# Optimization experiments

Hardware: AMD Instinct MI355X
Metric: run time of the kernel (lower is better)

Reference implementation:

```python
import math
import jax, jax.numpy as jnp
import numpy as np

B, S, HID = 2, 2048, 1024
NH, DQ, DV = 16, 64, 64

def _alibi_bias(n_heads, maxlen):
    # standard ALiBi slopes: 2^(-8*(h+1)/n_heads)
    slopes = jnp.asarray([2.0 ** (-8.0 * (h + 1) / n_heads) for h in range(n_heads)], dtype=jnp.float32)
    pos = jnp.arange(maxlen, dtype=jnp.float32)
    rel = pos[None, :] - pos[:, None]              # [i, j] = j - i  (<= 0 on causal part)
    return slopes[:, None, None] * rel[None]       # [n_heads, maxlen, maxlen]

def setup_inputs() -> dict:
    key = jax.random.key(0)
    ks = jax.random.split(key, 6)
    scale = 0.02
    return {
        "hidden_states": jax.random.normal(ks[0], (B, S, HID), dtype=jnp.float32),
        "attention_mask": jnp.ones((B, S), dtype=jnp.int32),
        "Wq": jax.random.normal(ks[1], (HID, NH * DQ), dtype=jnp.float32) * scale,
        "Wk": jax.random.normal(ks[2], (HID, NH * DQ), dtype=jnp.float32) * scale,
        "Wv": jax.random.normal(ks[3], (HID, NH * DV), dtype=jnp.float32) * scale,
        "Wo": jax.random.normal(ks[4], (NH * DV, HID), dtype=jnp.float32) * scale,
        "bo": jnp.zeros((HID,), dtype=jnp.float32),
        "alibi": _alibi_bias(NH, S),
    }

def reference(hidden_states, attention_mask, Wq, Wk, Wv, Wo, bo, alibi):
    N, t, _ = hidden_states.shape
    # QKV projections (no bias), split into heads: [N, H, t, d]
    q = (hidden_states @ Wq).reshape(N, t, NH, DQ).transpose(0, 2, 1, 3)
    k = (hidden_states @ Wk).reshape(N, t, NH, DQ).transpose(0, 2, 1, 3)
    v = (hidden_states @ Wv).reshape(N, t, NH, DV).transpose(0, 2, 1, 3)
    # raw scores, then ALiBi added BEFORE the 1/sqrt(d) scaling (as in source)
    scores = jnp.einsum("bhid,bhjd->bhij", q, k)
    scores = scores + alibi[None, :, :t, :t]
    scores = scores / math.sqrt(DQ)
    # grok tanh softcap at 30
    scores = 30.0 * jnp.tanh(scores / 30.0)
    # causal + padding masks
    causal = jnp.tril(jnp.ones((t, t), dtype=bool))
    scores = jnp.where(causal[None, None], scores, -jnp.inf)
    pad = (attention_mask != 0)[:, None, None, :]  # [N,1,1,T]
    scores = jnp.where(pad, scores, -jnp.inf)
    probs = jax.nn.softmax(scores, axis=-1)        # dropout p=0.0 (eval)
    ctx = jnp.einsum("bhij,bhjd->bhid", probs, v)
    ctx = ctx.transpose(0, 2, 1, 3).reshape(N, t, NH * DV)
    out = ctx @ Wo + bo
    return out
```

## Files before the change

### kernel.cpp

```cpp
#include <hip/hip_runtime.h>
#include <stdint.h>

#define BB 2
#define SS 2048
#define HID 1024
#define NHEAD 16
#define DHEAD 64
#define MTOT (BB*SS)

typedef float  f32x4  __attribute__((ext_vector_type(4)));
typedef short  s16x8  __attribute__((ext_vector_type(8)));
typedef unsigned short u16x4 __attribute__((ext_vector_type(4)));

#define LOG2E 1.4426950408889634f

__device__ __forceinline__ unsigned short f2bf(float x){
  union { float f; unsigned u; } v; v.f = x;
  unsigned r = v.u + 0x7fffu + ((v.u >> 16) & 1u);
  return (unsigned short)(r >> 16);
}

__device__ __forceinline__ void gl2lds16(const unsigned short* g, unsigned short* l){
  __builtin_amdgcn_global_load_lds((const __attribute__((address_space(1))) void*)g,
                                   (__attribute__((address_space(3))) void*)l, 16, 0, 0);
}

__global__ __launch_bounds__(256) void k_convert_x(const float* __restrict__ x,
                                                   unsigned short* __restrict__ xb){
  int i = blockIdx.x * 256 + threadIdx.x;
  const float4* xp = (const float4*)x;
  float4 v = xp[i];
  u16x4 o; o.x = f2bf(v.x); o.y = f2bf(v.y); o.z = f2bf(v.z); o.w = f2bf(v.w);
  ((u16x4*)xb)[i] = o;
}

__global__ __launch_bounds__(256) void k_convert_w(const float* __restrict__ Wq,
                                                   const float* __restrict__ Wk,
                                                   const float* __restrict__ Wv,
                                                   const float* __restrict__ Wo,
                                                   unsigned short* __restrict__ Wt,
                                                   unsigned short* __restrict__ Wot){
  __shared__ float tile[64][65];
  int z = blockIdx.z;
  const float* src = (z==0) ? Wq : (z==1) ? Wk : (z==2) ? Wv : Wo;
  unsigned short* dst = (z < 3) ? (Wt + z * HID * HID) : Wot;
  int n0 = blockIdx.x * 64, k0 = blockIdx.y * 64;
  int t = threadIdx.x, tx = t & 63, ty = t >> 6;
  #pragma unroll
  for (int i = 0; i < 16; i++){
    int kl = ty + i*4;
    tile[kl][tx] = src[(k0 + kl) * HID + n0 + tx];
  }
  __syncthreads();
  #pragma unroll
  for (int i = 0; i < 16; i++){
    int nl = ty + i*4;
    dst[(n0 + nl) * HID + k0 + tx] = f2bf(tile[tx][nl]);
  }
}

__global__ __launch_bounds__(256) void k_gemm_qkv(const unsigned short* __restrict__ A,
                                                  const unsigned short* __restrict__ Bt,
                                                  unsigned short* __restrict__ Qb,
                                                  unsigned short* __restrict__ Kb,
                                                  unsigned short* __restrict__ Vt){
  __shared__ __align__(16) unsigned short As[128*32];
  __shared__ __align__(16) unsigned short Bs[128*32];
  int t = threadIdx.x;
  int L = t & 63, w = t >> 6;
  int q = L >> 4, c = L & 15;
  int m0 = blockIdx.x * 128, n0 = blockIdx.y * 128;
  int wr = w >> 1, wc = w & 1;
  f32x4 acc[4][4];
  #pragma unroll
  for (int i = 0; i < 4; i++)
    #pragma unroll
    for (int j = 0; j < 4; j++) acc[i][j] = (f32x4){0.f,0.f,0.f,0.f};

  for (int kb = 0; kb < 32; kb++){
    __syncthreads();
    #pragma unroll
    for (int i = 0; i < 2; i++){
      int p = t + i*256;
      int row = p >> 2, cp = p & 3;
      gl2lds16(A  + (m0 + row) * HID + kb*32 + cp*8, As + p*8);
      gl2lds16(Bt + (n0 + row) * HID + kb*32 + cp*8, Bs + p*8);
    }
    __syncthreads();
    s16x8 af[4], bf[4];
    #pragma unroll
    for (int i = 0; i < 4; i++){
      int m = wr*64 + i*16 + c;
      af[i] = *(const s16x8*)(As + m*32 + q*8);
      int n = wc*64 + i*16 + c;
      bf[i] = *(const s16x8*)(Bs + n*32 + q*8);
    }
    #pragma unroll
    for (int i = 0; i < 4; i++)
      #pragma unroll
      for (int j = 0; j < 4; j++)
        acc[i][j] = __builtin_amdgcn_mfma_f32_16x16x32_bf16(af[i], bf[j], acc[i][j], 0, 0, 0);
  }

  int wsel = n0 >> 10;
  #pragma unroll
  for (int i = 0; i < 4; i++){
    #pragma unroll
    for (int j = 0; j < 4; j++){
      int m_l = wr*64 + i*16 + q*4;
      int n_g = n0 + wc*64 + j*16 + c;
      int nw  = n_g & 1023;
      if (wsel == 0){
        #pragma unroll
        for (int r = 0; r < 4; r++)
          Qb[(m0 + m_l + r) * HID + nw] = f2bf(acc[i][j][r] * 0.125f);
      } else if (wsel == 1){
        #pragma unroll
        for (int r = 0; r < 4; r++)
          Kb[(m0 + m_l + r) * HID + nw] = f2bf(acc[i][j][r]);
      } else {
        int tok = m0 + m_l;
        int b = tok >> 11, s = tok & 2047;
        int h = nw >> 6, d = nw & 63;
        u16x4 pk;
        pk.x = f2bf(acc[i][j][0]); pk.y = f2bf(acc[i][j][1]);
        pk.z = f2bf(acc[i][j][2]); pk.w = f2bf(acc[i][j][3]);
        *(u16x4*)(Vt + (((b*NHEAD + h)*DHEAD + d) * (size_t)SS + s)) = pk;
      }
    }
  }
}

__global__ __launch_bounds__(256) void k_attn(const unsigned short* __restrict__ Qb,
                                              const unsigned short* __restrict__ Kb,
                                              const unsigned short* __restrict__ Vt,
                                              const int* __restrict__ amask,
                                              unsigned short* __restrict__ ctx){
  __shared__ __align__(16) unsigned short UQ[4*16*72];
  __shared__ __align__(16) unsigned short Ks[64*64];
  __shared__ __align__(16) unsigned short Vs[64*64];

  int t = threadIdx.x;
  int L = t & 63, w = t >> 6;
  int q = L >> 4, c = L & 15;
  int qt = 31 - (int)blockIdx.x;
  int bh = blockIdx.y;
  int b = bh >> 4, h = bh & 15;
  int i0 = qt * 64;

  int hp = h + 1;
  float slope = (hp & 1) ? 0.70710678118654752f : 1.0f;
  slope = ldexpf(slope, -((hp >> 1) + 3));

  #pragma unroll
  for (int i = 0; i < 2; i++){
    int p = t + i*256; int row = p >> 3, cp = p & 7; int gc = cp ^ (row & 7);
    gl2lds16(Qb + (size_t)(b*SS + i0 + row) * HID + h*DHEAD + gc*8, UQ + p*8);
  }
  __syncthreads();
  s16x8 qf0, qf1;
  {
    int m = w*16 + c;
    qf0 = *(const s16x8*)(UQ + m*64 + ((0 + q) ^ (m & 7)) * 8);
    qf1 = *(const s16x8*)(UQ + m*64 + ((4 + q) ^ (m & 7)) * 8);
  }

  f32x4 cacc[4];
  #pragma unroll
  for (int i = 0; i < 4; i++) cacc[i] = (f32x4){0.f,0.f,0.f,0.f};
  float lrow[4] = {0.f,0.f,0.f,0.f};

  const float C1 = 86.5617024533378f;
  const float C2 = 0.0961796693925976f;

  for (int jt = 0; jt <= qt; jt++){
    int j0 = jt * 64;
    __syncthreads();
    #pragma unroll
    for (int i = 0; i < 2; i++){
      int p = t + i*256; int row = p >> 3, cp = p & 7; int gc = cp ^ (row & 7);
      gl2lds16(Kb + (size_t)(b*SS + j0 + row) * HID + h*DHEAD + gc*8, Ks + p*8);
      gl2lds16(Vt + (size_t)(bh*DHEAD + row) * SS + j0 + gc*8, Vs + p*8);
    }
    __syncthreads();

    f32x4 sacc[4];
    #pragma unroll
    for (int ct = 0; ct < 4; ct++){
      int n = ct*16 + c;
      s16x8 kf0 = *(const s16x8*)(Ks + n*64 + ((0 + q) ^ (n & 7)) * 8);
      s16x8 kf1 = *(const s16x8*)(Ks + n*64 + ((4 + q) ^ (n & 7)) * 8);
      f32x4 z = (f32x4){0.f,0.f,0.f,0.f};
      z = __builtin_amdgcn_mfma_f32_16x16x32_bf16(qf0, kf0, z, 0, 0, 0);
      z = __builtin_amdgcn_mfma_f32_16x16x32_bf16(qf1, kf1, z, 0, 0, 0);
      sacc[ct] = z;
    }

    float p_[4][4];
    #pragma unroll
    for (int ct = 0; ct < 4; ct++){
      int jg = j0 + ct*16 + c;
      int pad = amask[b*SS + jg];
      #pragma unroll
      for (int r = 0; r < 4; r++){
        int ig = i0 + w*16 + q*4 + r;
        float s = sacc[ct][r] + slope * (float)(jg - ig);
        float e2 = exp2f(s * C2);
        float pv = exp2f(-C1 / (e2 + 1.0f));
        bool ok = (jg <= ig) && (pad != 0);
        pv = ok ? pv : 0.0f;
        p_[ct][r] = pv;
        lrow[r] += pv;
      }
    }

    unsigned short* pw = UQ + w * (16*72);
    #pragma unroll
    for (int ct = 0; ct < 4; ct++)
      #pragma unroll
      for (int r = 0; r < 4; r++)
        pw[(q*4 + r)*72 + ct*16 + c] = f2bf(p_[ct][r]);

    s16x8 pf0 = *(const s16x8*)(pw + c*72 + q*8);
    s16x8 pf1 = *(const s16x8*)(pw + c*72 + 32 + q*8);
    #pragma unroll
    for (int nt = 0; nt < 4; nt++){
      int d = nt*16 + c;
      s16x8 vf0 = *(const s16x8*)(Vs + d*64 + ((0 + q) ^ (d & 7)) * 8);
      s16x8 vf1 = *(const s16x8*)(Vs + d*64 + ((4 + q) ^ (d & 7)) * 8);
      cacc[nt] = __builtin_amdgcn_mfma_f32_16x16x32_bf16(pf0, vf0, cacc[nt], 0, 0, 0);
      cacc[nt] = __builtin_amdgcn_mfma_f32_16x16x32_bf16(pf1, vf1, cacc[nt], 0, 0, 0);
    }
  }

  float inv[4];
  #pragma unroll
  for (int r = 0; r < 4; r++){
    float l = lrow[r];
    l += __shfl_xor(l, 1, 64);
    l += __shfl_xor(l, 2, 64);
    l += __shfl_xor(l, 4, 64);
    l += __shfl_xor(l, 8, 64);
    inv[r] = 1.0f / l;
  }
  #pragma unroll
  for (int nt = 0; nt < 4; nt++){
    int d = nt*16 + c;
    #pragma unroll
    for (int r = 0; r < 4; r++){
      int ig = i0 + w*16 + q*4 + r;
      ctx[(size_t)(b*SS + ig) * HID + h*DHEAD + d] = f2bf(cacc[nt][r] * inv[r]);
    }
  }
}

__global__ __launch_bounds__(256) void k_gemm_out(const unsigned short* __restrict__ A,
                                                  const unsigned short* __restrict__ Bt,
                                                  float* __restrict__ out,
                                                  const float* __restrict__ bo){
  __shared__ __align__(16) unsigned short As[128*32];
  __shared__ __align__(16) unsigned short Bs[128*32];
  int t = threadIdx.x;
  int L = t & 63, w = t >> 6;
  int q = L >> 4, c = L & 15;
  int m0 = blockIdx.x * 128, n0 = blockIdx.y * 128;
  int wr = w >> 1, wc = w & 1;
  f32x4 acc[4][4];
  #pragma unroll
  for (int i = 0; i < 4; i++)
    #pragma unroll
    for (int j = 0; j < 4; j++) acc[i][j] = (f32x4){0.f,0.f,0.f,0.f};

  for (int kb = 0; kb < 32; kb++){
    __syncthreads();
    #pragma unroll
    for (int i = 0; i < 2; i++){
      int p = t + i*256;
      int row = p >> 2, cp = p & 3;
      gl2lds16(A  + (m0 + row) * HID + kb*32 + cp*8, As + p*8);
      gl2lds16(Bt + (n0 + row) * HID + kb*32 + cp*8, Bs + p*8);
    }
    __syncthreads();
    s16x8 af[4], bf[4];
    #pragma unroll
    for (int i = 0; i < 4; i++){
      int m = wr*64 + i*16 + c;
      af[i] = *(const s16x8*)(As + m*32 + q*8);
      int n = wc*64 + i*16 + c;
      bf[i] = *(const s16x8*)(Bs + n*32 + q*8);
    }
    #pragma unroll
    for (int i = 0; i < 4; i++)
      #pragma unroll
      for (int j = 0; j < 4; j++)
        acc[i][j] = __builtin_amdgcn_mfma_f32_16x16x32_bf16(af[i], bf[j], acc[i][j], 0, 0, 0);
  }

  #pragma unroll
  for (int j = 0; j < 4; j++){
    int n = n0 + wc*64 + j*16 + c;
    float bv = bo[n];
    #pragma unroll
    for (int i = 0; i < 4; i++){
      int m = m0 + wr*64 + i*16 + q*4;
      #pragma unroll
      for (int r = 0; r < 4; r++)
        out[(size_t)(m + r) * HID + n] = acc[i][j][r] + bv;
    }
  }
}

extern "C" void kernel_launch(void* const* d_in, const int* in_sizes, int n_in,
                              void* d_out, int out_size, void* d_ws, size_t ws_size,
                              hipStream_t stream){
  const float* hs    = (const float*)d_in[0];
  const int*   amask = (const int*)  d_in[1];
  const float* Wq    = (const float*)d_in[2];
  const float* Wk    = (const float*)d_in[3];
  const float* Wv    = (const float*)d_in[4];
  const float* Wo    = (const float*)d_in[5];
  const float* bo    = (const float*)d_in[6];
  float* out = (float*)d_out;

  char* ws = (char*)d_ws;
  unsigned short* Xb  = (unsigned short*)(ws);
  unsigned short* Wt  = (unsigned short*)(ws + (8u  << 20));
  unsigned short* Wot = (unsigned short*)(ws + (14u << 20));
  unsigned short* Qb  = (unsigned short*)(ws + (16u << 20));
  unsigned short* Kb  = (unsigned short*)(ws + (24u << 20));
  unsigned short* Vt  = (unsigned short*)(ws + (32u << 20));
  unsigned short* Ctx = (unsigned short*)(ws + (40u << 20));

  hipLaunchKernelGGL(k_convert_x, dim3(MTOT*HID/4/256), dim3(256), 0, stream, hs, Xb);
  hipLaunchKernelGGL(k_convert_w, dim3(16,16,4), dim3(256), 0, stream, Wq, Wk, Wv, Wo, Wt, Wot);
  hipLaunchKernelGGL(k_gemm_qkv,  dim3(32,24),   dim3(256), 0, stream, Xb, Wt, Qb, Kb, Vt);
  hipLaunchKernelGGL(k_attn,      dim3(32,32),   dim3(256), 0, stream, Qb, Kb, Vt, amask, Ctx);
  hipLaunchKernelGGL(k_gemm_out,  dim3(32,8),    dim3(256), 0, stream, Ctx, Wot, out, bo);
}
```

Before: 555.5 us.

## Split long causal attention rows across two blocks and combine partial sums

The attention grid grows from 32 to 48 query-tile slots per head. The upper 16 query tiles, which have the longest causal key ranges, are each split into two key chunks handled by separate blocks. This balances the work across blocks. Partial numerators and row sums are written to workspace and merged in a new combine kernel that also normalises. The change also moves the V transpose out of the QKV GEMM epilogue into its own kernel, applies the causal mask only on the diagonal tile, and uses a hardware reciprocal. The cost is extra launches, fp32 partial traffic, and bf16 rounding of the unnormalised numerator.

```diff
diff --git a/kernel.cpp b/kernel.cpp
--- a/kernel.cpp
+++ b/kernel.cpp
@@ -18,6 +18,9 @@
   union { float f; unsigned u; } v; v.f = x;
   unsigned r = v.u + 0x7fffu + ((v.u >> 16) & 1u);
   return (unsigned short)(r >> 16);
+}
+__device__ __forceinline__ float bf2f(unsigned short h){
+  union { unsigned u; float f; } v; v.u = ((unsigned)h) << 16; return v.f;
 }
 
 __device__ __forceinline__ void gl2lds16(const unsigned short* g, unsigned short* l){
@@ -63,7 +66,7 @@
                                                   const unsigned short* __restrict__ Bt,
                                                   unsigned short* __restrict__ Qb,
                                                   unsigned short* __restrict__ Kb,
-                                                  unsigned short* __restrict__ Vt){
+                                                  unsigned short* __restrict__ Vb){
   __shared__ __align__(16) unsigned short As[128*32];
   __shared__ __align__(16) unsigned short Bs[128*32];
   int t = threadIdx.x;
@@ -103,31 +106,46 @@
   }
 
   int wsel = n0 >> 10;
+  unsigned short* dst = (wsel==0) ? Qb : (wsel==1) ? Kb : Vb;
+  float scale = (wsel==0) ? 0.125f : 1.0f;
   #pragma unroll
   for (int i = 0; i < 4; i++){
     #pragma unroll
     for (int j = 0; j < 4; j++){
       int m_l = wr*64 + i*16 + q*4;
-      int n_g = n0 + wc*64 + j*16 + c;
-      int nw  = n_g & 1023;
-      if (wsel == 0){
-        #pragma unroll
-        for (int r = 0; r < 4; r++)
-          Qb[(m0 + m_l + r) * HID + nw] = f2bf(acc[i][j][r] * 0.125f);
-      } else if (wsel == 1){
-        #pragma unroll
-        for (int r = 0; r < 4; r++)
-          Kb[(m0 + m_l + r) * HID + nw] = f2bf(acc[i][j][r]);
-      } else {
-        int tok = m0 + m_l;
-        int b = tok >> 11, s = tok & 2047;
-        int h = nw >> 6, d = nw & 63;
-        u16x4 pk;
-        pk.x = f2bf(acc[i][j][0]); pk.y = f2bf(acc[i][j][1]);
-        pk.z = f2bf(acc[i][j][2]); pk.w = f2bf(acc[i][j][3]);
-        *(u16x4*)(Vt + (((b*NHEAD + h)*DHEAD + d) * (size_t)SS + s)) = pk;
-      }
-    }
+      int nw  = (n0 + wc*64 + j*16 + c) & 1023;
+      #pragma unroll
+      for (int r = 0; r < 4; r++)
+        dst[(m0 + m_l + r) * HID + nw] = f2bf(acc[i][j][r] * scale);
+    }
+  }
+}
+
+__global__ __launch_bounds__(256) void k_transpose_v(const unsigned short* __restrict__ Vb,
+                                                     unsigned short* __restrict__ Vt){
+  __shared__ unsigned tile[64][33];
+  int st = blockIdx.x, bh = blockIdx.y;
+  int b = bh >> 4, h = bh & 15;
+  int t = threadIdx.x;
+  int lr = t >> 4, lc = t & 15;
+  #pragma unroll
+  for (int i = 0; i < 4; i++){
+    int sl = lr + i*16;
+    u16x4 v = *(const u16x4*)(Vb + (size_t)(b*SS + st*64 + sl) * HID + h*DHEAD + lc*4);
+    tile[sl][lc*2]     = (unsigned)v.x | ((unsigned)v.y << 16);
+    tile[sl][lc*2 + 1] = (unsigned)v.z | ((unsigned)v.w << 16);
+  }
+  __syncthreads();
+  #pragma unroll
+  for (int i = 0; i < 4; i++){
+    int dl = lr + i*16;
+    int sh = (dl & 1) * 16, dw = dl >> 1;
+    u16x4 o;
+    o.x = (unsigned short)(tile[lc*4 + 0][dw] >> sh);
+    o.y = (unsigned short)(tile[lc*4 + 1][dw] >> sh);
+    o.z = (unsigned short)(tile[lc*4 + 2][dw] >> sh);
+    o.w = (unsigned short)(tile[lc*4 + 3][dw] >> sh);
+    *(u16x4*)(Vt + (size_t)(bh*DHEAD + dl) * SS + st*64 + lc*4) = o;
   }
 }
 
@@ -135,7 +153,10 @@
                                               const unsigned short* __restrict__ Kb,
                                               const unsigned short* __restrict__ Vt,
                                               const int* __restrict__ amask,
-                                              unsigned short* __restrict__ ctx){
+                                              unsigned short* __restrict__ NumBf,
+                                              float* __restrict__ Lsum,
+                                              float* __restrict__ Part2,
+                                              float* __restrict__ L2){
   __shared__ __align__(16) unsigned short UQ[4*16*72];
   __shared__ __align__(16) unsigned short Ks[64*64];
   __shared__ __align__(16) unsigned short Vs[64*64];
@@ -143,9 +164,21 @@
   int t = threadIdx.x;
   int L = t & 63, w = t >> 6;
   int q = L >> 4, c = L & 15;
-  int qt = 31 - (int)blockIdx.x;
+  int x = blockIdx.x;
   int bh = blockIdx.y;
   int b = bh >> 4, h = bh & 15;
+
+  int qt, jt0, jt1, chunk1;
+  if (x < 32){
+    qt = 31 - (x >> 1);
+    int h0 = (qt + 1) >> 1;
+    chunk1 = x & 1;
+    jt0 = chunk1 ? h0 : 0;
+    jt1 = chunk1 ? (qt + 1) : h0;
+  } else {
+    qt = 47 - x;
+    jt0 = 0; jt1 = qt + 1; chunk1 = 0;
+  }
   int i0 = qt * 64;
 
   int hp = h + 1;
@@ -165,6 +198,10 @@
     qf1 = *(const s16x8*)(UQ + m*64 + ((4 + q) ^ (m & 7)) * 8);
   }
 
+  float si[4];
+  #pragma unroll
+  for (int r = 0; r < 4; r++) si[r] = slope * (float)(i0 + w*16 + q*4 + r);
+
   f32x4 cacc[4];
   #pragma unroll
   for (int i = 0; i < 4; i++) cacc[i] = (f32x4){0.f,0.f,0.f,0.f};
@@ -173,7 +210,7 @@
   const float C1 = 86.5617024533378f;
   const float C2 = 0.0961796693925976f;
 
-  for (int jt = 0; jt <= qt; jt++){
+  for (int jt = jt0; jt < jt1; jt++){
     int j0 = jt * 64;
     __syncthreads();
     #pragma unroll
@@ -200,19 +237,31 @@
     #pragma unroll
     for (int ct = 0; ct < 4; ct++){
       int jg = j0 + ct*16 + c;
-      int pad = amask[b*SS + jg];
+      float padf = (amask[b*SS + jg] != 0) ? 1.0f : 0.0f;
+      float sjg = slope * (float)jg;
       #pragma unroll
       for (int r = 0; r < 4; r++){
-        int ig = i0 + w*16 + q*4 + r;
-        float s = sacc[ct][r] + slope * (float)(jg - ig);
+        float s = sacc[ct][r] + (sjg - si[r]);
         float e2 = exp2f(s * C2);
-        float pv = exp2f(-C1 / (e2 + 1.0f));
-        bool ok = (jg <= ig) && (pad != 0);
-        pv = ok ? pv : 0.0f;
-        p_[ct][r] = pv;
-        lrow[r] += pv;
+        float pv = exp2f(-C1 * __builtin_amdgcn_rcpf(e2 + 1.0f));
+        p_[ct][r] = pv * padf;
       }
     }
+    if (jt == qt){
+      #pragma unroll
+      for (int ct = 0; ct < 4; ct++){
+        int jg = j0 + ct*16 + c;
+        #pragma unroll
+        for (int r = 0; r < 4; r++){
+          int ig = i0 + w*16 + q*4 + r;
+          if (jg > ig) p_[ct][r] = 0.0f;
+        }
+      }
+    }
+    #pragma unroll
+    for (int ct = 0; ct < 4; ct++)
+      #pragma unroll
+      for (int r = 0; r < 4; r++) lrow[r] += p_[ct][r];
 
     unsigned short* pw = UQ + w * (16*72);
     #pragma unroll
@@ -233,7 +282,7 @@
     }
   }
 
-  float inv[4];
+  float lred[4];
   #pragma unroll
   for (int r = 0; r < 4; r++){
     float l = lrow[r];
@@ -241,17 +290,67 @@
     l += __shfl_xor(l, 2, 64);
     l += __shfl_xor(l, 4, 64);
     l += __shfl_xor(l, 8, 64);
-    inv[r] = 1.0f / l;
-  }
-  #pragma unroll
-  for (int nt = 0; nt < 4; nt++){
-    int d = nt*16 + c;
-    #pragma unroll
-    for (int r = 0; r < 4; r++){
-      int ig = i0 + w*16 + q*4 + r;
-      ctx[(size_t)(b*SS + ig) * HID + h*DHEAD + d] = f2bf(cacc[nt][r] * inv[r]);
-    }
-  }
+    lred[r] = l;
+  }
+
+  if (!chunk1){
+    #pragma unroll
+    for (int nt = 0; nt < 4; nt++){
+      int d = nt*16 + c;
+      #pragma unroll
+      for (int r = 0; r < 4; r++){
+        int ig = i0 + w*16 + q*4 + r;
+        NumBf[(size_t)(b*SS + ig) * HID + h*DHEAD + d] = f2bf(cacc[nt][r]);
+      }
+    }
+    if (c == 0){
+      #pragma unroll
+      for (int r = 0; r < 4; r++)
+        Lsum[bh*SS + i0 + w*16 + q*4 + r] = lred[r];
+    }
+  } else {
+    int slot = bh*16 + (qt - 16);
+    float* pn = Part2 + (size_t)slot * 64 * 64;
+    #pragma unroll
+    for (int nt = 0; nt < 4; nt++){
+      int d = nt*16 + c;
+      #pragma unroll
+      for (int r = 0; r < 4; r++){
+        int row = w*16 + q*4 + r;
+        pn[row*64 + d] = cacc[nt][r];
+      }
+    }
+    if (c == 0){
+      #pragma unroll
+      for (int r = 0; r < 4; r++)
+        L2[slot*64 + w*16 + q*4 + r] = lred[r];
+    }
+  }
+}
+
+__global__ __launch_bounds__(256) void k_combine(unsigned short* __restrict__ NumBf,
+                                                 const float* __restrict__ Lsum,
+                                                 const float* __restrict__ Part2,
+                                                 const float* __restrict__ L2){
+  int idx = blockIdx.x * 256 + threadIdx.x;
+  int tok = idx >> 8;
+  int hd4 = (idx & 255) * 4;
+  int h = hd4 >> 6, d0 = hd4 & 63;
+  int b = tok >> 11, i = tok & 2047;
+  int bh = b*16 + h, qt = i >> 6;
+  u16x4 nv = *(u16x4*)(NumBf + (size_t)tok * HID + hd4);
+  float n0 = bf2f(nv.x), n1 = bf2f(nv.y), n2 = bf2f(nv.z), n3 = bf2f(nv.w);
+  float l = Lsum[bh*SS + i];
+  if (qt >= 16){
+    int slot = bh*16 + (qt - 16);
+    const float* pn = Part2 + ((size_t)slot * 64 + (i & 63)) * 64 + d0;
+    n0 += pn[0]; n1 += pn[1]; n2 += pn[2]; n3 += pn[3];
+    l += L2[slot*64 + (i & 63)];
+  }
+  float rl = __builtin_amdgcn_rcpf(l);
+  u16x4 o;
+  o.x = f2bf(n0*rl); o.y = f2bf(n1*rl); o.z = f2bf(n2*rl); o.w = f2bf(n3*rl);
+  *(u16x4*)(NumBf + (size_t)tok * HID + hd4) = o;
 }
 
 __global__ __launch_bounds__(256) void k_gemm_out(const unsigned short* __restrict__ A,
@@ -330,10 +429,17 @@
   unsigned short* Kb  = (unsigned short*)(ws + (24u << 20));
   unsigned short* Vt  = (unsigned short*)(ws + (32u << 20));
   unsigned short* Ctx = (unsigned short*)(ws + (40u << 20));
-
-  hipLaunchKernelGGL(k_convert_x, dim3(MTOT*HID/4/256), dim3(256), 0, stream, hs, Xb);
-  hipLaunchKernelGGL(k_convert_w, dim3(16,16,4), dim3(256), 0, stream, Wq, Wk, Wv, Wo, Wt, Wot);
-  hipLaunchKernelGGL(k_gemm_qkv,  dim3(32,24),   dim3(256), 0, stream, Xb, Wt, Qb, Kb, Vt);
-  hipLaunchKernelGGL(k_attn,      dim3(32,32),   dim3(256), 0, stream, Qb, Kb, Vt, amask, Ctx);
-  hipLaunchKernelGGL(k_gemm_out,  dim3(32,8),    dim3(256), 0, stream, Ctx, Wot, out, bo);
-}
+  float* Part2 = (float*)(ws);
+  float* L2    = (float*)(ws + (8u << 20));
+  float* Lsum  = (float*)(ws + (8u << 20) + (512u << 10));
+  unsigned short* Vb = Ctx;
+
+  hipLaunchKernelGGL(k_convert_x,  dim3(MTOT*HID/4/256), dim3(256), 0, stream, hs, Xb);
+  hipLaunchKernelGGL(k_convert_w,  dim3(16,16,4), dim3(256), 0, stream, Wq, Wk, Wv, Wo, Wt, Wot);
+  hipLaunchKernelGGL(k_gemm_qkv,   dim3(32,24),   dim3(256), 0, stream, Xb, Wt, Qb, Kb, Vb);
+  hipLaunchKernelGGL(k_transpose_v,dim3(32,32),   dim3(256), 0, stream, Vb, Vt);
+  hipLaunchKernelGGL(k_attn,       dim3(48,32),   dim3(256), 0, stream, Qb, Kb, Vt, amask,
+                                   Ctx, Lsum, Part2, L2);
+  hipLaunchKernelGGL(k_combine,    dim3(MTOT*HID/4/256), dim3(256), 0, stream, Ctx, Lsum, Part2, L2);
+  hipLaunchKernelGGL(k_gemm_out,   dim3(32,8),    dim3(256), 0, stream, Ctx, Wot, out, bo);
+}
```

Result: faster. 471.9 us (-15.0%).
